# Kernel tuning notes

Hardware: AMD Instinct MI355X
Metric: run time of the kernel (lower is better)

The kernel has to match this reference:

```python
import jax, jax.numpy as jnp
import numpy as np

N = 40000      # nodes
E = 640000     # edges (avg degree 16)
ND = 128       # node_dim
ED = 64        # edge_dim
LN_EPS = 1e-5


def setup_inputs() -> dict:
    key = jax.random.key(0)
    ks = jax.random.split(key, 16)
    s = lambda k, shape, fan_in: jax.random.normal(k, shape, dtype=jnp.float32) * (1.0 / np.sqrt(fan_in))
    return {
        "node_features": jax.random.normal(ks[0], (N, ND), dtype=jnp.float32),
        "edge_indices": jax.random.randint(ks[1], (2, E), 0, N, dtype=jnp.int32),
        "edge_features": jax.random.normal(ks[2], (E, ED), dtype=jnp.float32),
        # message_mlp: Linear(2*ND+ED -> ND), LayerNorm(ND), ReLU, Linear(ND -> ND)
        "W1": s(ks[3], (2 * ND + ED, ND), 2 * ND + ED),
        "b1": jnp.zeros((ND,), jnp.float32),
        "ln_g": jnp.ones((ND,), jnp.float32),
        "ln_b": jnp.zeros((ND,), jnp.float32),
        "W2": s(ks[4], (ND, ND), ND),
        "b2": jnp.zeros((ND,), jnp.float32),
        # edge_gate: Linear(ED -> 1) + Sigmoid
        "gate_w": s(ks[5], (ED, 1), ED),
        "gate_b": jnp.zeros((1,), jnp.float32),
        # GRUCell(ND, ND): weight_ih [3*ND, ND], weight_hh [3*ND, ND] (gates r, z, n)
        "W_ih": s(ks[6], (3 * ND, ND), ND),
        "b_ih": jnp.zeros((3 * ND,), jnp.float32),
        "W_hh": s(ks[7], (3 * ND, ND), ND),
        "b_hh": jnp.zeros((3 * ND,), jnp.float32),
    }


def reference(node_features, edge_indices, edge_features, W1, b1, ln_g, ln_b,
              W2, b2, gate_w, gate_b, W_ih, b_ih, W_hh, b_hh):
    src, dst = edge_indices[0], edge_indices[1]
    # gather src/dst node features and concat with edge features -> [E, 2*ND+ED]
    edge_inputs = jnp.concatenate(
        [node_features[src], node_features[dst], edge_features], axis=1)
    # message MLP: Linear -> LayerNorm -> ReLU -> Linear
    h = edge_inputs @ W1 + b1
    mu = jnp.mean(h, axis=-1, keepdims=True)
    var = jnp.var(h, axis=-1, keepdims=True)
    h = (h - mu) * jax.lax.rsqrt(var + LN_EPS) * ln_g + ln_b
    h = jax.nn.relu(h)
    messages = h @ W2 + b2                                   # [E, ND]
    # sigmoid edge gate from raw edge features
    gate = jax.nn.sigmoid(edge_features @ gate_w + gate_b)   # [E, 1]
    messages = messages * gate
    # scatter-add into destination nodes
    agg = jax.ops.segment_sum(messages, dst, num_segments=node_features.shape[0])
    # GRUCell(input=agg, hidden=node_features), torch gate order: r, z, n
    gi = agg @ W_ih.T + b_ih
    gh = node_features @ W_hh.T + b_hh
    i_r, i_z, i_n = jnp.split(gi, 3, axis=1)
    h_r, h_z, h_n = jnp.split(gh, 3, axis=1)
    r = jax.nn.sigmoid(i_r + h_r)
    z = jax.nn.sigmoid(i_z + h_z)
    n = jnp.tanh(i_n + r * h_n)
    return (1.0 - z) * n + z * node_features
```

## Files before the change

### kernel.cpp

```cpp
#include <hip/hip_runtime.h>
#include <math.h>

#define ND 128
#define ED 64
#define LN_EPS 1e-5f
#define TE 64
#define SXH 328
#define GSH 136
#define GSF 132

typedef _Float16 f16;
typedef __attribute__((ext_vector_type(8))) _Float16 f16x8;
typedef __attribute__((ext_vector_type(4))) _Float16 f16x4;
typedef __attribute__((ext_vector_type(4))) float f32x4;

__device__ __forceinline__ float sigmoidf_(float x) { return 1.f / (1.f + expf(-x)); }

__global__ void convert_kernel(const float* __restrict__ W1, const float* __restrict__ W2,
                               const float* __restrict__ Wih, const float* __restrict__ Whh,
                               f16* __restrict__ W1f, f16* __restrict__ W2f,
                               f16* __restrict__ Wihf, f16* __restrict__ Whhf)
{
    int idx = blockIdx.x * 256 + threadIdx.x;
    if (idx < 40960) {
        int n = idx / 320, k = idx - n * 320;
        W1f[idx] = (f16)W1[k * 128 + n];
    } else if (idx < 57344) {
        int i2 = idx - 40960; int n = i2 >> 7, k = i2 & 127;
        W2f[i2] = (f16)W2[k * 128 + n];
    } else if (idx < 106496) {
        int i3 = idx - 57344;  Wihf[i3] = (f16)Wih[i3];
    } else if (idx < 155648) {
        int i4 = idx - 106496; Whhf[i4] = (f16)Whh[i4];
    }
}

__global__ void nf16_kernel(const float* __restrict__ nf, f16* __restrict__ nf16, int n8) {
    int i = blockIdx.x * 256 + threadIdx.x;
    if (i < n8) {
        float4 a = ((const float4*)nf)[2 * i];
        float4 b = ((const float4*)nf)[2 * i + 1];
        f16x8 h;
        h[0] = (f16)a.x; h[1] = (f16)a.y; h[2] = (f16)a.z; h[3] = (f16)a.w;
        h[4] = (f16)b.x; h[5] = (f16)b.y; h[6] = (f16)b.z; h[7] = (f16)b.w;
        ((f16x8*)nf16)[i] = h;
    }
}

__global__ void hist_kernel(const int* __restrict__ eidx, int* __restrict__ cnt, int E) {
    int i = blockIdx.x * 256 + threadIdx.x;
    if (i < E) atomicAdd(&cnt[eidx[E + i]], 1);
}

__global__ __launch_bounds__(1024)
void scan_kernel(const int* __restrict__ cnt, int* __restrict__ woff, int N) {
    __shared__ int part[1024];
    const int t = threadIdx.x;
    const int CH = 40;
    int base = t * CH;
    int s = 0;
    for (int i = 0; i < CH; ++i) { int idx = base + i; if (idx < N) s += cnt[idx]; }
    part[t] = s;
    __syncthreads();
    for (int d = 1; d < 1024; d <<= 1) {
        int v = (t >= d) ? part[t - d] : 0;
        __syncthreads();
        part[t] += v;
        __syncthreads();
    }
    int run = (t == 0) ? 0 : part[t - 1];
    for (int i = 0; i < CH; ++i) {
        int idx = base + i;
        if (idx < N) { woff[idx] = run; run += cnt[idx]; }
    }
}

__global__ void scatter_kernel(const int* __restrict__ eidx, int* __restrict__ woff,
                               int* __restrict__ perm, int E) {
    int i = blockIdx.x * 256 + threadIdx.x;
    if (i < E) {
        int p = atomicAdd(&woff[eidx[E + i]], 1);
        perm[p] = i;
    }
}

__global__ __launch_bounds__(256, 3)
void edge_kernel(const f16* __restrict__ nf16, const int* __restrict__ eidx,
                 const float* __restrict__ ef, const int* __restrict__ perm,
                 const f16* __restrict__ W1f, const float* __restrict__ b1,
                 const float* __restrict__ ln_g, const float* __restrict__ ln_b,
                 const f16* __restrict__ W2f, const float* __restrict__ b2,
                 const float* __restrict__ gate_w, const float* __restrict__ gate_b,
                 float* __restrict__ agg, int E)
{
    __shared__ f16   sxh[TE * SXH];
    __shared__ float sred[TE * 8];
    __shared__ float spart[TE][4];
    __shared__ float sg[TE];
    __shared__ int   se_s[TE], ssrc_s[TE], sdst_s[TE];

    const int tid  = threadIdx.x;
    const int lane = tid & 63;
    const int w    = __builtin_amdgcn_readfirstlane(tid >> 6);
    const int cb   = 32 * w;
    const int c    = lane & 15;
    const int quad = lane >> 4;
    const int e0   = blockIdx.x * TE;

    if (tid < TE) {
        int e = perm[e0 + tid];
        se_s[tid]   = e;
        ssrc_s[tid] = eidx[e];
        sdst_s[tid] = eidx[E + e];
    }
    __syncthreads();

    {
        const int r = tid >> 2, q = tid & 3;
        const f16*   srow = nf16 + (size_t)ssrc_s[r] * ND;
        const f16*   drow = nf16 + (size_t)sdst_s[r] * ND;
        const float* erow = ef + (size_t)se_s[r] * ED;
        f16* dp = sxh + r * SXH;
        #pragma unroll
        for (int i = 0; i < 4; ++i) {
            int ch = (q + 4 * i) * 8;
            *(f16x8*)(dp + ch)       = *(const f16x8*)(srow + ch);
            *(f16x8*)(dp + 128 + ch) = *(const f16x8*)(drow + ch);
        }
        float gp = 0.f;
        #pragma unroll
        for (int i = 0; i < 4; ++i) {
            int ec = (q + 4 * i) * 4;
            float4 v = *(const float4*)(erow + ec);
            f16x4 h4; h4[0] = (f16)v.x; h4[1] = (f16)v.y; h4[2] = (f16)v.z; h4[3] = (f16)v.w;
            *(f16x4*)(dp + 256 + ec) = h4;
            const float* gw = gate_w + ec;
            gp = fmaf(v.x, gw[0], gp); gp = fmaf(v.y, gw[1], gp);
            gp = fmaf(v.z, gw[2], gp); gp = fmaf(v.w, gw[3], gp);
        }
        spart[r][q] = gp;
    }
    __syncthreads();

    if (tid < TE)
        sg[tid] = sigmoidf_(spart[tid][0] + spart[tid][1] + spart[tid][2] + spart[tid][3] + gate_b[0]);

    f32x4 acc[4][2];
    #pragma unroll
    for (int mt = 0; mt < 4; ++mt)
        #pragma unroll
        for (int nt = 0; nt < 2; ++nt) acc[mt][nt] = (f32x4){0.f, 0.f, 0.f, 0.f};

    #pragma unroll
    for (int ks = 0; ks < 10; ++ks) {
        f16x8 b0 = *(const f16x8*)(W1f + (cb + c) * 320 + ks * 32 + quad * 8);
        f16x8 b1v = *(const f16x8*)(W1f + (cb + 16 + c) * 320 + ks * 32 + quad * 8);
        #pragma unroll
        for (int mt = 0; mt < 4; ++mt) {
            f16x8 a = *(const f16x8*)(sxh + (16 * mt + c) * SXH + ks * 32 + quad * 8);
            acc[mt][0] = __builtin_amdgcn_mfma_f32_16x16x32_f16(a, b0,  acc[mt][0], 0, 0, 0);
            acc[mt][1] = __builtin_amdgcn_mfma_f32_16x16x32_f16(a, b1v, acc[mt][1], 0, 0, 0);
        }
    }

    float b1c[2], gvc[2], bvc[2], b2c[2];
    #pragma unroll
    for (int nt = 0; nt < 2; ++nt) {
        int col = cb + nt * 16 + c;
        b1c[nt] = b1[col]; gvc[nt] = ln_g[col]; bvc[nt] = ln_b[col]; b2c[nt] = b2[col];
    }
    #pragma unroll
    for (int mt = 0; mt < 4; ++mt) {
        float p1[4] = {0, 0, 0, 0}, p2[4] = {0, 0, 0, 0};
        #pragma unroll
        for (int nt = 0; nt < 2; ++nt)
            #pragma unroll
            for (int r = 0; r < 4; ++r) {
                float vv = acc[mt][nt][r] + b1c[nt];
                acc[mt][nt][r] = vv;
                p1[r] += vv; p2[r] += vv * vv;
            }
        #pragma unroll
        for (int m = 1; m < 16; m <<= 1)
            #pragma unroll
            for (int r = 0; r < 4; ++r) {
                p1[r] += __shfl_xor(p1[r], m);
                p2[r] += __shfl_xor(p2[r], m);
            }
        if (c == 0) {
            #pragma unroll
            for (int r = 0; r < 4; ++r) {
                int row = 16 * mt + 4 * quad + r;
                sred[row * 8 + 2 * w + 0] = p1[r];
                sred[row * 8 + 2 * w + 1] = p2[r];
            }
        }
    }
    __syncthreads();

    #pragma unroll
    for (int mt = 0; mt < 4; ++mt)
        #pragma unroll
        for (int r = 0; r < 4; ++r) {
            int row = 16 * mt + 4 * quad + r;
            f32x4 lo = *(const f32x4*)(sred + row * 8);
            f32x4 hi = *(const f32x4*)(sred + row * 8 + 4);
            float t1 = lo[0] + lo[2] + hi[0] + hi[2];
            float t2 = lo[1] + lo[3] + hi[1] + hi[3];
            float mu = t1 * (1.f / 128.f);
            float var = t2 * (1.f / 128.f) - mu * mu;
            float rs = rsqrtf(var + LN_EPS);
            #pragma unroll
            for (int nt = 0; nt < 2; ++nt) {
                float vv = (acc[mt][nt][r] - mu) * rs * gvc[nt] + bvc[nt];
                vv = vv > 0.f ? vv : 0.f;
                sxh[row * SXH + cb + nt * 16 + c] = (f16)vv;
            }
        }
    __syncthreads();

    f32x4 acc2[4][2];
    #pragma unroll
    for (int mt = 0; mt < 4; ++mt)
        #pragma unroll
        for (int nt = 0; nt < 2; ++nt) acc2[mt][nt] = (f32x4){0.f, 0.f, 0.f, 0.f};
    #pragma unroll
    for (int ks = 0; ks < 4; ++ks) {
        f16x8 b0 = *(const f16x8*)(W2f + (cb + c) * 128 + ks * 32 + quad * 8);
        f16x8 b1v = *(const f16x8*)(W2f + (cb + 16 + c) * 128 + ks * 32 + quad * 8);
        #pragma unroll
        for (int mt = 0; mt < 4; ++mt) {
            f16x8 a = *(const f16x8*)(sxh + (16 * mt + c) * SXH + ks * 32 + quad * 8);
            acc2[mt][0] = __builtin_amdgcn_mfma_f32_16x16x32_f16(a, b0,  acc2[mt][0], 0, 0, 0);
            acc2[mt][1] = __builtin_amdgcn_mfma_f32_16x16x32_f16(a, b1v, acc2[mt][1], 0, 0, 0);
        }
    }
    __syncthreads();

    float* smsg = (float*)sxh;
    #pragma unroll
    for (int mt = 0; mt < 4; ++mt)
        #pragma unroll
        for (int r = 0; r < 4; ++r) {
            int row = 16 * mt + 4 * quad + r;
            float gr = sg[row];
            #pragma unroll
            for (int nt = 0; nt < 2; ++nt)
                smsg[row * 164 + cb + nt * 16 + c] = (acc2[mt][nt][r] + b2c[nt]) * gr;
        }
    __syncthreads();

    {
        const int rbase = 16 * w;
        const float* sm = smsg + rbase * 164;
        float run0 = sm[lane];
        float run1 = sm[64 + lane];
        int prev = __builtin_amdgcn_readfirstlane(sdst_s[rbase]);
        #pragma unroll
        for (int r = 1; r < 16; ++r) {
            int d = __builtin_amdgcn_readfirstlane(sdst_s[rbase + r]);
            float v0 = sm[r * 164 + lane];
            float v1 = sm[r * 164 + 64 + lane];
            if (d == prev) { run0 += v0; run1 += v1; }
            else {
                atomicAdd(agg + (size_t)prev * ND + lane,      run0);
                atomicAdd(agg + (size_t)prev * ND + 64 + lane, run1);
                run0 = v0; run1 = v1; prev = d;
            }
        }
        atomicAdd(agg + (size_t)prev * ND + lane,      run0);
        atomicAdd(agg + (size_t)prev * ND + 64 + lane, run1);
    }
}

__global__ __launch_bounds__(256, 2)
void gru_kernel(const float* __restrict__ agg, const float* __restrict__ nf,
                const f16* __restrict__ Wihf, const float* __restrict__ b_ih,
                const f16* __restrict__ Whhf, const float* __restrict__ b_hh,
                float* __restrict__ out)
{
    __shared__ f16   sa[32 * GSH];
    __shared__ f16   sh[32 * GSH];
    __shared__ float shf[32 * GSF];

    const int tid  = threadIdx.x;
    const int lane = tid & 63;
    const int w    = __builtin_amdgcn_readfirstlane(tid >> 6);
    const int c    = lane & 15;
    const int quad = lane >> 4;
    const int n0   = blockIdx.x * 32;

    {
        const int r = tid >> 3, q = tid & 7;
        const float* arow = agg + (size_t)(n0 + r) * ND;
        const float* hrow = nf  + (size_t)(n0 + r) * ND;
        #pragma unroll
        for (int i = 0; i < 4; ++i) {
            int ec = (q + 8 * i) * 4;
            float4 va = *(const float4*)(arow + ec);
            f16x4 ha; ha[0] = (f16)va.x; ha[1] = (f16)va.y; ha[2] = (f16)va.z; ha[3] = (f16)va.w;
            *(f16x4*)(sa + r * GSH + ec) = ha;
            float4 vh = *(const float4*)(hrow + ec);
            f16x4 hh; hh[0] = (f16)vh.x; hh[1] = (f16)vh.y; hh[2] = (f16)vh.z; hh[3] = (f16)vh.w;
            *(f16x4*)(sh + r * GSH + ec) = hh;
            *(float4*)(shf + r * GSF + ec) = vh;
        }
    }
    __syncthreads();

    f32x4 aI[2][6], aH[2][6];
    #pragma unroll
    for (int mt = 0; mt < 2; ++mt)
        #pragma unroll
        for (int j = 0; j < 6; ++j) {
            aI[mt][j] = (f32x4){0.f, 0.f, 0.f, 0.f};
            aH[mt][j] = (f32x4){0.f, 0.f, 0.f, 0.f};
        }

    #pragma unroll
    for (int ks = 0; ks < 4; ++ks) {
        f16x8 fa[2], fh[2];
        #pragma unroll
        for (int mt = 0; mt < 2; ++mt) {
            fa[mt] = *(const f16x8*)(sa + (16 * mt + c) * GSH + ks * 32 + quad * 8);
            fh[mt] = *(const f16x8*)(sh + (16 * mt + c) * GSH + ks * 32 + quad * 8);
        }
        #pragma unroll
        for (int gg = 0; gg < 3; ++gg)
            #pragma unroll
            for (int nt = 0; nt < 2; ++nt) {
                int coln = gg * 128 + 32 * w + nt * 16 + c;
                f16x8 bI = *(const f16x8*)(Wihf + coln * 128 + ks * 32 + quad * 8);
                f16x8 bH = *(const f16x8*)(Whhf + coln * 128 + ks * 32 + quad * 8);
                #pragma unroll
                for (int mt = 0; mt < 2; ++mt) {
                    int j = gg * 2 + nt;
                    aI[mt][j] = __builtin_amdgcn_mfma_f32_16x16x32_f16(fa[mt], bI, aI[mt][j], 0, 0, 0);
                    aH[mt][j] = __builtin_amdgcn_mfma_f32_16x16x32_f16(fh[mt], bH, aH[mt][j], 0, 0, 0);
                }
            }
    }

    #pragma unroll
    for (int nt = 0; nt < 2; ++nt) {
        int col = 32 * w + nt * 16 + c;
        float bir = b_ih[col], biz = b_ih[128 + col], bin = b_ih[256 + col];
        float bhr = b_hh[col], bhz = b_hh[128 + col], bhn = b_hh[256 + col];
        #pragma unroll
        for (int mt = 0; mt < 2; ++mt)
            #pragma unroll
            for (int r = 0; r < 4; ++r) {
                int row = 16 * mt + 4 * quad + r;
                float rr = sigmoidf_(aI[mt][0 + nt][r] + bir + aH[mt][0 + nt][r] + bhr);
                float zz = sigmoidf_(aI[mt][2 + nt][r] + biz + aH[mt][2 + nt][r] + bhz);
                float nn = tanhf(aI[mt][4 + nt][r] + bin + rr * (aH[mt][4 + nt][r] + bhn));
                float hp = shf[row * GSF + col];
                out[(size_t)(n0 + row) * ND + col] = (1.f - zz) * nn + zz * hp;
            }
    }
}

extern "C" void kernel_launch(void* const* d_in, const int* in_sizes, int n_in,
                              void* d_out, int out_size, void* d_ws, size_t ws_size,
                              hipStream_t stream) {
    const float* nf     = (const float*)d_in[0];
    const int*   eidx   = (const int*)  d_in[1];
    const float* ef     = (const float*)d_in[2];
    const float* W1     = (const float*)d_in[3];
    const float* b1     = (const float*)d_in[4];
    const float* ln_g   = (const float*)d_in[5];
    const float* ln_b   = (const float*)d_in[6];
    const float* W2     = (const float*)d_in[7];
    const float* b2     = (const float*)d_in[8];
    const float* gate_w = (const float*)d_in[9];
    const float* gate_b = (const float*)d_in[10];
    const float* W_ih   = (const float*)d_in[11];
    const float* b_ih   = (const float*)d_in[12];
    const float* W_hh   = (const float*)d_in[13];
    const float* b_hh   = (const float*)d_in[14];
    float* out = (float*)d_out;

    const int N = in_sizes[0] / ND;
    const int E = in_sizes[1] / 2;

    char* ws = (char*)d_ws;
    float* agg = (float*)ws;          ws += (size_t)N * ND * 4;
    f16* nf16 = (f16*)ws;             ws += (size_t)N * ND * 2;
    f16* W1f  = (f16*)ws;             ws += 40960 * 2;
    f16* W2f  = (f16*)ws;             ws += 16384 * 2;
    f16* Wihf = (f16*)ws;             ws += 49152 * 2;
    f16* Whhf = (f16*)ws;             ws += 49152 * 2;
    int* cnt  = (int*)ws;             ws += 40960 * 4;
    int* woff = (int*)ws;             ws += 40960 * 4;
    int* perm = (int*)ws;             ws += (size_t)E * 4;

    hipMemsetAsync(agg, 0, (size_t)N * ND * 4, stream);
    hipMemsetAsync(cnt, 0, (size_t)N * 4, stream);
    convert_kernel<<<608, 256, 0, stream>>>(W1, W2, W_ih, W_hh, W1f, W2f, Wihf, Whhf);
    const int n8 = N * ND / 8;
    nf16_kernel<<<(n8 + 255) / 256, 256, 0, stream>>>(nf, nf16, n8);
    hist_kernel<<<(E + 255) / 256, 256, 0, stream>>>(eidx, cnt, E);
    scan_kernel<<<1, 1024, 0, stream>>>(cnt, woff, N);
    scatter_kernel<<<(E + 255) / 256, 256, 0, stream>>>(eidx, woff, perm, E);
    edge_kernel<<<E / TE, 256, 0, stream>>>(nf16, eidx, ef, perm, W1f, b1, ln_g, ln_b,
                                            W2f, b2, gate_w, gate_b, agg, E);
    gru_kernel<<<N / 32, 256, 0, stream>>>(agg, nf, Wihf, b_ih, Whhf, b_hh, out);
}
```

Measured before the change: 611.6 us.

## Halve edge tile, gather node rows via global_load_lds, fuse nf16 conversion into convert

Shrinks the edge tile from 64 to 32 edges per block and raises the occupancy hint from 3 to 5 blocks per SM. Source and destination node rows are now copied straight into LDS with global_load_lds, with indices held in registers and broadcast via readlane instead of staged through shared arrays, which removes one barrier. The node-feature fp16 conversion is folded into the weight-conversion kernel, saving a launch. Smaller tiles mean each W1/W2 fragment loaded from global memory feeds fewer MFMAs, and segmented reduction runs over 8 rows per wave, so more atomics may be issued.

After: 701.3 us. 1.15x slower.

```diff
diff --git a/kernel.cpp b/kernel.cpp
--- a/kernel.cpp
+++ b/kernel.cpp
@@ -4,7 +4,7 @@
 #define ND 128
 #define ED 64
 #define LN_EPS 1e-5f
-#define TE 64
+#define TE 32
 #define SXH 328
 #define GSH 136
 #define GSF 132
@@ -14,12 +14,18 @@
 typedef __attribute__((ext_vector_type(4))) _Float16 f16x4;
 typedef __attribute__((ext_vector_type(4))) float f32x4;
 
+#define GLD4(gp, lp) __builtin_amdgcn_global_load_lds( \
+    (const __attribute__((address_space(1))) void*)(gp), \
+    (__attribute__((address_space(3))) void*)(lp), 4, 0, 0)
+
 __device__ __forceinline__ float sigmoidf_(float x) { return 1.f / (1.f + expf(-x)); }
 
 __global__ void convert_kernel(const float* __restrict__ W1, const float* __restrict__ W2,
                                const float* __restrict__ Wih, const float* __restrict__ Whh,
+                               const float* __restrict__ nf,
                                f16* __restrict__ W1f, f16* __restrict__ W2f,
-                               f16* __restrict__ Wihf, f16* __restrict__ Whhf)
+                               f16* __restrict__ Wihf, f16* __restrict__ Whhf,
+                               f16* __restrict__ nf16, int n8)
 {
     int idx = blockIdx.x * 256 + threadIdx.x;
     if (idx < 40960) {
@@ -32,18 +38,16 @@
         int i3 = idx - 57344;  Wihf[i3] = (f16)Wih[i3];
     } else if (idx < 155648) {
         int i4 = idx - 106496; Whhf[i4] = (f16)Whh[i4];
-    }
-}
-
-__global__ void nf16_kernel(const float* __restrict__ nf, f16* __restrict__ nf16, int n8) {
-    int i = blockIdx.x * 256 + threadIdx.x;
-    if (i < n8) {
-        float4 a = ((const float4*)nf)[2 * i];
-        float4 b = ((const float4*)nf)[2 * i + 1];
-        f16x8 h;
-        h[0] = (f16)a.x; h[1] = (f16)a.y; h[2] = (f16)a.z; h[3] = (f16)a.w;
-        h[4] = (f16)b.x; h[5] = (f16)b.y; h[6] = (f16)b.z; h[7] = (f16)b.w;
-        ((f16x8*)nf16)[i] = h;
+    } else {
+        int i5 = idx - 155648;
+        if (i5 < n8) {
+            float4 a = ((const float4*)nf)[2 * i5];
+            float4 b = ((const float4*)nf)[2 * i5 + 1];
+            f16x8 h;
+            h[0] = (f16)a.x; h[1] = (f16)a.y; h[2] = (f16)a.z; h[3] = (f16)a.w;
+            h[4] = (f16)b.x; h[5] = (f16)b.y; h[6] = (f16)b.z; h[7] = (f16)b.w;
+            ((f16x8*)nf16)[i5] = h;
+        }
     }
 }
 
@@ -84,7 +88,7 @@
     }
 }
 
-__global__ __launch_bounds__(256, 3)
+__global__ __launch_bounds__(256, 5)
 void edge_kernel(const f16* __restrict__ nf16, const int* __restrict__ eidx,
                  const float* __restrict__ ef, const int* __restrict__ perm,
                  const f16* __restrict__ W1f, const float* __restrict__ b1,
@@ -95,9 +99,8 @@
 {
     __shared__ f16   sxh[TE * SXH];
     __shared__ float sred[TE * 8];
-    __shared__ float spart[TE][4];
+    __shared__ float spart[TE][8];
     __shared__ float sg[TE];
-    __shared__ int   se_s[TE], ssrc_s[TE], sdst_s[TE];
 
     const int tid  = threadIdx.x;
     const int lane = tid & 63;
@@ -107,47 +110,52 @@
     const int quad = lane >> 4;
     const int e0   = blockIdx.x * TE;
 
+    int ev = 0, sr = 0, dr = 0;
+    if (lane < 32) {
+        ev = perm[e0 + lane];
+        sr = eidx[ev];
+        dr = eidx[E + ev];
+    }
+
+    #pragma unroll
+    for (int i = 0; i < 8; ++i) {
+        int r = 8 * w + i;
+        int srcr = __builtin_amdgcn_readlane(sr, r);
+        int drr  = __builtin_amdgcn_readlane(dr, r);
+        GLD4(nf16 + (size_t)srcr * ND + 2 * lane, sxh + r * SXH);
+        GLD4(nf16 + (size_t)drr  * ND + 2 * lane, sxh + r * SXH + 128);
+    }
+
+    {
+        const int r = tid >> 3, q = tid & 7;
+        int er = __shfl(ev, r);
+        const float* erow = ef + (size_t)er * ED + q * 8;
+        float4 v0 = *(const float4*)erow;
+        float4 v1 = *(const float4*)(erow + 4);
+        f16x4 h0; h0[0] = (f16)v0.x; h0[1] = (f16)v0.y; h0[2] = (f16)v0.z; h0[3] = (f16)v0.w;
+        f16x4 h1; h1[0] = (f16)v1.x; h1[1] = (f16)v1.y; h1[2] = (f16)v1.z; h1[3] = (f16)v1.w;
+        f16* dp = sxh + r * SXH + 256 + q * 8;
+        *(f16x4*)dp = h0;
+        *(f16x4*)(dp + 4) = h1;
+        const float* gw = gate_w + q * 8;
+        float gp = 0.f;
+        gp = fmaf(v0.x, gw[0], gp); gp = fmaf(v0.y, gw[1], gp);
+        gp = fmaf(v0.z, gw[2], gp); gp = fmaf(v0.w, gw[3], gp);
+        gp = fmaf(v1.x, gw[4], gp); gp = fmaf(v1.y, gw[5], gp);
+        gp = fmaf(v1.z, gw[6], gp); gp = fmaf(v1.w, gw[7], gp);
+        spart[r][q] = gp;
+    }
+    __syncthreads();
+
     if (tid < TE) {
-        int e = perm[e0 + tid];
-        se_s[tid]   = e;
-        ssrc_s[tid] = eidx[e];
-        sdst_s[tid] = eidx[E + e];
-    }
-    __syncthreads();
-
-    {
-        const int r = tid >> 2, q = tid & 3;
-        const f16*   srow = nf16 + (size_t)ssrc_s[r] * ND;
-        const f16*   drow = nf16 + (size_t)sdst_s[r] * ND;
-        const float* erow = ef + (size_t)se_s[r] * ED;
-        f16* dp = sxh + r * SXH;
-        #pragma unroll
-        for (int i = 0; i < 4; ++i) {
-            int ch = (q + 4 * i) * 8;
-            *(f16x8*)(dp + ch)       = *(const f16x8*)(srow + ch);
-            *(f16x8*)(dp + 128 + ch) = *(const f16x8*)(drow + ch);
-        }
-        float gp = 0.f;
-        #pragma unroll
-        for (int i = 0; i < 4; ++i) {
-            int ec = (q + 4 * i) * 4;
-            float4 v = *(const float4*)(erow + ec);
-            f16x4 h4; h4[0] = (f16)v.x; h4[1] = (f16)v.y; h4[2] = (f16)v.z; h4[3] = (f16)v.w;
-            *(f16x4*)(dp + 256 + ec) = h4;
-            const float* gw = gate_w + ec;
-            gp = fmaf(v.x, gw[0], gp); gp = fmaf(v.y, gw[1], gp);
-            gp = fmaf(v.z, gw[2], gp); gp = fmaf(v.w, gw[3], gp);
-        }
-        spart[r][q] = gp;
-    }
-    __syncthreads();
-
-    if (tid < TE)
-        sg[tid] = sigmoidf_(spart[tid][0] + spart[tid][1] + spart[tid][2] + spart[tid][3] + gate_b[0]);
-
-    f32x4 acc[4][2];
-    #pragma unroll
-    for (int mt = 0; mt < 4; ++mt)
+        float s = spart[tid][0] + spart[tid][1] + spart[tid][2] + spart[tid][3]
+                + spart[tid][4] + spart[tid][5] + spart[tid][6] + spart[tid][7];
+        sg[tid] = sigmoidf_(s + gate_b[0]);
+    }
+
+    f32x4 acc[2][2];
+    #pragma unroll
+    for (int mt = 0; mt < 2; ++mt)
         #pragma unroll
         for (int nt = 0; nt < 2; ++nt) acc[mt][nt] = (f32x4){0.f, 0.f, 0.f, 0.f};
 
@@ -156,7 +164,7 @@
         f16x8 b0 = *(const f16x8*)(W1f + (cb + c) * 320 + ks * 32 + quad * 8);
         f16x8 b1v = *(const f16x8*)(W1f + (cb + 16 + c) * 320 + ks * 32 + quad * 8);
         #pragma unroll
-        for (int mt = 0; mt < 4; ++mt) {
+        for (int mt = 0; mt < 2; ++mt) {
             f16x8 a = *(const f16x8*)(sxh + (16 * mt + c) * SXH + ks * 32 + quad * 8);
             acc[mt][0] = __builtin_amdgcn_mfma_f32_16x16x32_f16(a, b0,  acc[mt][0], 0, 0, 0);
             acc[mt][1] = __builtin_amdgcn_mfma_f32_16x16x32_f16(a, b1v, acc[mt][1], 0, 0, 0);
@@ -170,7 +178,7 @@
         b1c[nt] = b1[col]; gvc[nt] = ln_g[col]; bvc[nt] = ln_b[col]; b2c[nt] = b2[col];
     }
     #pragma unroll
-    for (int mt = 0; mt < 4; ++mt) {
+    for (int mt = 0; mt < 2; ++mt) {
         float p1[4] = {0, 0, 0, 0}, p2[4] = {0, 0, 0, 0};
         #pragma unroll
         for (int nt = 0; nt < 2; ++nt)
@@ -199,7 +207,7 @@
     __syncthreads();
 
     #pragma unroll
-    for (int mt = 0; mt < 4; ++mt)
+    for (int mt = 0; mt < 2; ++mt)
         #pragma unroll
         for (int r = 0; r < 4; ++r) {
             int row = 16 * mt + 4 * quad + r;
@@ -219,9 +227,9 @@
         }
     __syncthreads();
 
-    f32x4 acc2[4][2];
-    #pragma unroll
-    for (int mt = 0; mt < 4; ++mt)
+    f32x4 acc2[2][2];
+    #pragma unroll
+    for (int mt = 0; mt < 2; ++mt)
         #pragma unroll
         for (int nt = 0; nt < 2; ++nt) acc2[mt][nt] = (f32x4){0.f, 0.f, 0.f, 0.f};
     #pragma unroll
@@ -229,7 +237,7 @@
         f16x8 b0 = *(const f16x8*)(W2f + (cb + c) * 128 + ks * 32 + quad * 8);
         f16x8 b1v = *(const f16x8*)(W2f + (cb + 16 + c) * 128 + ks * 32 + quad * 8);
         #pragma unroll
-        for (int mt = 0; mt < 4; ++mt) {
+        for (int mt = 0; mt < 2; ++mt) {
             f16x8 a = *(const f16x8*)(sxh + (16 * mt + c) * SXH + ks * 32 + quad * 8);
             acc2[mt][0] = __builtin_amdgcn_mfma_f32_16x16x32_f16(a, b0,  acc2[mt][0], 0, 0, 0);
             acc2[mt][1] = __builtin_amdgcn_mfma_f32_16x16x32_f16(a, b1v, acc2[mt][1], 0, 0, 0);
@@ -239,7 +247,7 @@
 
     float* smsg = (float*)sxh;
     #pragma unroll
-    for (int mt = 0; mt < 4; ++mt)
+    for (int mt = 0; mt < 2; ++mt)
         #pragma unroll
         for (int r = 0; r < 4; ++r) {
             int row = 16 * mt + 4 * quad + r;
@@ -251,14 +259,14 @@
     __syncthreads();
 
     {
-        const int rbase = 16 * w;
+        const int rbase = 8 * w;
         const float* sm = smsg + rbase * 164;
         float run0 = sm[lane];
         float run1 = sm[64 + lane];
-        int prev = __builtin_amdgcn_readfirstlane(sdst_s[rbase]);
-        #pragma unroll
-        for (int r = 1; r < 16; ++r) {
-            int d = __builtin_amdgcn_readfirstlane(sdst_s[rbase + r]);
+        int prev = __builtin_amdgcn_readlane(dr, rbase);
+        #pragma unroll
+        for (int r = 1; r < 8; ++r) {
+            int d = __builtin_amdgcn_readlane(dr, rbase + r);
             float v0 = sm[r * 164 + lane];
             float v1 = sm[r * 164 + 64 + lane];
             if (d == prev) { run0 += v0; run1 += v1; }
@@ -396,9 +404,10 @@
 
     hipMemsetAsync(agg, 0, (size_t)N * ND * 4, stream);
     hipMemsetAsync(cnt, 0, (size_t)N * 4, stream);
-    convert_kernel<<<608, 256, 0, stream>>>(W1, W2, W_ih, W_hh, W1f, W2f, Wihf, Whhf);
     const int n8 = N * ND / 8;
-    nf16_kernel<<<(n8 + 255) / 256, 256, 0, stream>>>(nf, nf16, n8);
+    const int cvt_items = 155648 + n8;
+    convert_kernel<<<(cvt_items + 255) / 256, 256, 0, stream>>>(
+        W1, W2, W_ih, W_hh, nf, W1f, W2f, Wihf, Whhf, nf16, n8);
     hist_kernel<<<(E + 255) / 256, 256, 0, stream>>>(eidx, cnt, E);
     scan_kernel<<<1, 1024, 0, stream>>>(cnt, woff, N);
     scatter_kernel<<<(E + 255) / 256, 256, 0, stream>>>(eidx, woff, perm, E);
```

## Precompute per-node W1 projections to shrink per-edge first GEMM

Applied to the files above, without the earlier changes.

Splits the first linear layer so the src and dst node parts are computed once per node (N×256 f16 table) in a new h12 kernel, and the edge kernel only gathers and sums two projected rows plus a K=64 edge-feature GEMM. This removes most of the per-edge first-layer MFMA work (K 320→64) and the separate nf16 conversion. Shared memory is reorganised with XOR swizzling and shrunk, and occupancy is raised to 4 blocks per CU. The risk is extra f16 rounding, since the projected values are stored in half precision and summed in f16 before the bias and LayerNorm.

After: 562.1 us. 8.1% less time.

```diff
diff --git a/kernel.cpp b/kernel.cpp
--- a/kernel.cpp
+++ b/kernel.cpp
@@ -5,7 +5,6 @@
 #define ED 64
 #define LN_EPS 1e-5f
 #define TE 64
-#define SXH 328
 #define GSH 136
 #define GSF 132
 
@@ -18,32 +17,83 @@
 
 __global__ void convert_kernel(const float* __restrict__ W1, const float* __restrict__ W2,
                                const float* __restrict__ Wih, const float* __restrict__ Whh,
-                               f16* __restrict__ W1f, f16* __restrict__ W2f,
+                               f16* __restrict__ Wcatf, f16* __restrict__ W1ef,
+                               f16* __restrict__ W2f,
                                f16* __restrict__ Wihf, f16* __restrict__ Whhf)
 {
     int idx = blockIdx.x * 256 + threadIdx.x;
-    if (idx < 40960) {
-        int n = idx / 320, k = idx - n * 320;
-        W1f[idx] = (f16)W1[k * 128 + n];
+    if (idx < 32768) {
+        int cc = idx >> 7, k = idx & 127;
+        Wcatf[idx] = (f16)(cc < 128 ? W1[k * 128 + cc] : W1[(128 + k) * 128 + (cc - 128)]);
+    } else if (idx < 40960) {
+        int i2 = idx - 32768; int n = i2 >> 6, k = i2 & 63;
+        W1ef[i2] = (f16)W1[(256 + k) * 128 + n];
     } else if (idx < 57344) {
-        int i2 = idx - 40960; int n = i2 >> 7, k = i2 & 127;
-        W2f[i2] = (f16)W2[k * 128 + n];
+        int i3 = idx - 40960; int n = i3 >> 7, k = i3 & 127;
+        W2f[i3] = (f16)W2[k * 128 + n];
     } else if (idx < 106496) {
-        int i3 = idx - 57344;  Wihf[i3] = (f16)Wih[i3];
+        int i4 = idx - 57344;  Wihf[i4] = (f16)Wih[i4];
     } else if (idx < 155648) {
-        int i4 = idx - 106496; Whhf[i4] = (f16)Whh[i4];
-    }
-}
-
-__global__ void nf16_kernel(const float* __restrict__ nf, f16* __restrict__ nf16, int n8) {
-    int i = blockIdx.x * 256 + threadIdx.x;
-    if (i < n8) {
-        float4 a = ((const float4*)nf)[2 * i];
-        float4 b = ((const float4*)nf)[2 * i + 1];
-        f16x8 h;
-        h[0] = (f16)a.x; h[1] = (f16)a.y; h[2] = (f16)a.z; h[3] = (f16)a.w;
-        h[4] = (f16)b.x; h[5] = (f16)b.y; h[6] = (f16)b.z; h[7] = (f16)b.w;
-        ((f16x8*)nf16)[i] = h;
+        int i5 = idx - 106496; Whhf[i5] = (f16)Whh[i5];
+    }
+}
+
+__global__ __launch_bounds__(256)
+void h12_kernel(const float* __restrict__ nf, const f16* __restrict__ Wcatf,
+                f16* __restrict__ H12f)
+{
+    __shared__ f16 sa[32 * GSH];
+    const int tid  = threadIdx.x;
+    const int lane = tid & 63;
+    const int w    = __builtin_amdgcn_readfirstlane(tid >> 6);
+    const int c    = lane & 15;
+    const int quad = lane >> 4;
+    const int n0   = blockIdx.x * 32;
+
+    {
+        const int r = tid >> 3, q = tid & 7;
+        const float* hrow = nf + (size_t)(n0 + r) * ND;
+        #pragma unroll
+        for (int i = 0; i < 4; ++i) {
+            int ec = (q + 8 * i) * 4;
+            float4 v = *(const float4*)(hrow + ec);
+            f16x4 h; h[0] = (f16)v.x; h[1] = (f16)v.y; h[2] = (f16)v.z; h[3] = (f16)v.w;
+            *(f16x4*)(sa + r * GSH + ec) = h;
+        }
+    }
+    __syncthreads();
+
+    f32x4 acc[2][4];
+    #pragma unroll
+    for (int mt = 0; mt < 2; ++mt)
+        #pragma unroll
+        for (int nt = 0; nt < 4; ++nt) acc[mt][nt] = (f32x4){0.f, 0.f, 0.f, 0.f};
+
+    #pragma unroll
+    for (int ks = 0; ks < 4; ++ks) {
+        f16x8 fa[2];
+        #pragma unroll
+        for (int mt = 0; mt < 2; ++mt)
+            fa[mt] = *(const f16x8*)(sa + (16 * mt + c) * GSH + ks * 32 + quad * 8);
+        #pragma unroll
+        for (int nt = 0; nt < 4; ++nt) {
+            f16x8 b = *(const f16x8*)(Wcatf + (64 * w + nt * 16 + c) * 128 + ks * 32 + quad * 8);
+            #pragma unroll
+            for (int mt = 0; mt < 2; ++mt)
+                acc[mt][nt] = __builtin_amdgcn_mfma_f32_16x16x32_f16(fa[mt], b, acc[mt][nt], 0, 0, 0);
+        }
+    }
+
+    #pragma unroll
+    for (int nt = 0; nt < 4; ++nt) {
+        int col = 64 * w + nt * 16 + c;
+        #pragma unroll
+        for (int mt = 0; mt < 2; ++mt)
+            #pragma unroll
+            for (int r = 0; r < 4; ++r) {
+                int row = 16 * mt + 4 * quad + r;
+                H12f[(size_t)(n0 + row) * 256 + col] = (f16)acc[mt][nt][r];
+            }
     }
 }
 
@@ -84,20 +134,23 @@
     }
 }
 
-__global__ __launch_bounds__(256, 3)
-void edge_kernel(const f16* __restrict__ nf16, const int* __restrict__ eidx,
+__global__ __launch_bounds__(256, 4)
+void edge_kernel(const f16* __restrict__ H12f, const int* __restrict__ eidx,
                  const float* __restrict__ ef, const int* __restrict__ perm,
-                 const f16* __restrict__ W1f, const float* __restrict__ b1,
+                 const f16* __restrict__ W1ef, const float* __restrict__ b1,
                  const float* __restrict__ ln_g, const float* __restrict__ ln_b,
                  const f16* __restrict__ W2f, const float* __restrict__ b2,
                  const float* __restrict__ gate_w, const float* __restrict__ gate_b,
                  float* __restrict__ agg, int E)
 {
-    __shared__ f16   sxh[TE * SXH];
+    __shared__ float smsg[TE * 128];
     __shared__ float sred[TE * 8];
     __shared__ float spart[TE][4];
     __shared__ float sg[TE];
     __shared__ int   se_s[TE], ssrc_s[TE], sdst_s[TE];
+
+    char* shb  = (char*)smsg;
+    char* sefb = (char*)smsg + 16384;
 
     const int tid  = threadIdx.x;
     const int lane = tid & 63;
@@ -117,26 +170,34 @@
 
     {
         const int r = tid >> 2, q = tid & 3;
-        const f16*   srow = nf16 + (size_t)ssrc_s[r] * ND;
-        const f16*   drow = nf16 + (size_t)sdst_s[r] * ND;
+        const f16* h1p = H12f + (size_t)ssrc_s[r] * 256;
+        const f16* h2p = H12f + (size_t)sdst_s[r] * 256 + 128;
+        const int swz = (r & 7) << 4;
+        #pragma unroll
+        for (int i = 0; i < 4; ++i) {
+            int ch = q + 4 * i;
+            f16x8 a = *(const f16x8*)(h1p + ch * 8);
+            f16x8 b = *(const f16x8*)(h2p + ch * 8);
+            f16x8 s = a + b;
+            *(f16x8*)(shb + ((r * 256 + ch * 16) ^ swz)) = s;
+        }
         const float* erow = ef + (size_t)se_s[r] * ED;
-        f16* dp = sxh + r * SXH;
-        #pragma unroll
-        for (int i = 0; i < 4; ++i) {
-            int ch = (q + 4 * i) * 8;
-            *(f16x8*)(dp + ch)       = *(const f16x8*)(srow + ch);
-            *(f16x8*)(dp + 128 + ch) = *(const f16x8*)(drow + ch);
-        }
         float gp = 0.f;
         #pragma unroll
-        for (int i = 0; i < 4; ++i) {
-            int ec = (q + 4 * i) * 4;
-            float4 v = *(const float4*)(erow + ec);
-            f16x4 h4; h4[0] = (f16)v.x; h4[1] = (f16)v.y; h4[2] = (f16)v.z; h4[3] = (f16)v.w;
-            *(f16x4*)(dp + 256 + ec) = h4;
-            const float* gw = gate_w + ec;
-            gp = fmaf(v.x, gw[0], gp); gp = fmaf(v.y, gw[1], gp);
-            gp = fmaf(v.z, gw[2], gp); gp = fmaf(v.w, gw[3], gp);
+        for (int j = 0; j < 2; ++j) {
+            int ch = 2 * q + j;
+            const float* p = erow + ch * 8;
+            float4 v0 = *(const float4*)p;
+            float4 v1 = *(const float4*)(p + 4);
+            f16x8 h;
+            h[0] = (f16)v0.x; h[1] = (f16)v0.y; h[2] = (f16)v0.z; h[3] = (f16)v0.w;
+            h[4] = (f16)v1.x; h[5] = (f16)v1.y; h[6] = (f16)v1.z; h[7] = (f16)v1.w;
+            *(f16x8*)(sefb + ((r * 128 + ch * 16) ^ swz)) = h;
+            const float* gw = gate_w + ch * 8;
+            gp = fmaf(v0.x, gw[0], gp); gp = fmaf(v0.y, gw[1], gp);
+            gp = fmaf(v0.z, gw[2], gp); gp = fmaf(v0.w, gw[3], gp);
+            gp = fmaf(v1.x, gw[4], gp); gp = fmaf(v1.y, gw[5], gp);
+            gp = fmaf(v1.z, gw[6], gp); gp = fmaf(v1.w, gw[7], gp);
         }
         spart[r][q] = gp;
     }
@@ -152,12 +213,12 @@
         for (int nt = 0; nt < 2; ++nt) acc[mt][nt] = (f32x4){0.f, 0.f, 0.f, 0.f};
 
     #pragma unroll
-    for (int ks = 0; ks < 10; ++ks) {
-        f16x8 b0 = *(const f16x8*)(W1f + (cb + c) * 320 + ks * 32 + quad * 8);
-        f16x8 b1v = *(const f16x8*)(W1f + (cb + 16 + c) * 320 + ks * 32 + quad * 8);
+    for (int ks = 0; ks < 2; ++ks) {
+        f16x8 b0 = *(const f16x8*)(W1ef + (cb + c) * 64 + ks * 32 + quad * 8);
+        f16x8 b1v = *(const f16x8*)(W1ef + (cb + 16 + c) * 64 + ks * 32 + quad * 8);
         #pragma unroll
         for (int mt = 0; mt < 4; ++mt) {
-            f16x8 a = *(const f16x8*)(sxh + (16 * mt + c) * SXH + ks * 32 + quad * 8);
+            f16x8 a = *(const f16x8*)(sefb + (((16 * mt + c) * 128 + ks * 64 + quad * 16) ^ ((c & 7) << 4)));
             acc[mt][0] = __builtin_amdgcn_mfma_f32_16x16x32_f16(a, b0,  acc[mt][0], 0, 0, 0);
             acc[mt][1] = __builtin_amdgcn_mfma_f32_16x16x32_f16(a, b1v, acc[mt][1], 0, 0, 0);
         }
@@ -176,7 +237,10 @@
         for (int nt = 0; nt < 2; ++nt)
             #pragma unroll
             for (int r = 0; r < 4; ++r) {
-                float vv = acc[mt][nt][r] + b1c[nt];
+                int row = 16 * mt + 4 * quad + r;
+                int col = cb + nt * 16 + c;
+                float h12v = (float)(*(const f16*)(shb + ((row * 256 + col * 2) ^ ((row & 7) << 4))));
+                float vv = acc[mt][nt][r] + b1c[nt] + h12v;
                 acc[mt][nt][r] = vv;
                 p1[r] += vv; p2[r] += vv * vv;
             }
@@ -212,9 +276,10 @@
             float rs = rsqrtf(var + LN_EPS);
             #pragma unroll
             for (int nt = 0; nt < 2; ++nt) {
+                int col = cb + nt * 16 + c;
                 float vv = (acc[mt][nt][r] - mu) * rs * gvc[nt] + bvc[nt];
                 vv = vv > 0.f ? vv : 0.f;
-                sxh[row * SXH + cb + nt * 16 + c] = (f16)vv;
+                *(f16*)(shb + ((row * 256 + col * 2) ^ ((row & 7) << 4))) = (f16)vv;
             }
         }
     __syncthreads();
@@ -230,14 +295,13 @@
         f16x8 b1v = *(const f16x8*)(W2f + (cb + 16 + c) * 128 + ks * 32 + quad * 8);
         #pragma unroll
         for (int mt = 0; mt < 4; ++mt) {
-            f16x8 a = *(const f16x8*)(sxh + (16 * mt + c) * SXH + ks * 32 + quad * 8);
+            f16x8 a = *(const f16x8*)(shb + (((16 * mt + c) * 256 + ks * 64 + quad * 16) ^ ((c & 7) << 4)));
             acc2[mt][0] = __builtin_amdgcn_mfma_f32_16x16x32_f16(a, b0,  acc2[mt][0], 0, 0, 0);
             acc2[mt][1] = __builtin_amdgcn_mfma_f32_16x16x32_f16(a, b1v, acc2[mt][1], 0, 0, 0);
         }
     }
     __syncthreads();
 
-    float* smsg = (float*)sxh;
     #pragma unroll
     for (int mt = 0; mt < 4; ++mt)
         #pragma unroll
@@ -245,22 +309,25 @@
             int row = 16 * mt + 4 * quad + r;
             float gr = sg[row];
             #pragma unroll
-            for (int nt = 0; nt < 2; ++nt)
-                smsg[row * 164 + cb + nt * 16 + c] = (acc2[mt][nt][r] + b2c[nt]) * gr;
+            for (int nt = 0; nt < 2; ++nt) {
+                int col = cb + nt * 16 + c;
+                smsg[(row * 128 + col) ^ ((row & 7) << 2)] = (acc2[mt][nt][r] + b2c[nt]) * gr;
+            }
         }
     __syncthreads();
 
     {
         const int rbase = 16 * w;
-        const float* sm = smsg + rbase * 164;
-        float run0 = sm[lane];
-        float run1 = sm[64 + lane];
-        int prev = __builtin_amdgcn_readfirstlane(sdst_s[rbase]);
+        int row0 = rbase;
+        float run0 = smsg[(row0 * 128 + lane) ^ ((row0 & 7) << 2)];
+        float run1 = smsg[(row0 * 128 + 64 + lane) ^ ((row0 & 7) << 2)];
+        int prev = sdst_s[rbase];
         #pragma unroll
         for (int r = 1; r < 16; ++r) {
-            int d = __builtin_amdgcn_readfirstlane(sdst_s[rbase + r]);
-            float v0 = sm[r * 164 + lane];
-            float v1 = sm[r * 164 + 64 + lane];
+            int row = rbase + r;
+            int d = sdst_s[row];
+            float v0 = smsg[(row * 128 + lane) ^ ((row & 7) << 2)];
+            float v1 = smsg[(row * 128 + 64 + lane) ^ ((row & 7) << 2)];
             if (d == prev) { run0 += v0; run1 += v1; }
             else {
                 atomicAdd(agg + (size_t)prev * ND + lane,      run0);
@@ -384,25 +451,26 @@
     const int E = in_sizes[1] / 2;
 
     char* ws = (char*)d_ws;
-    float* agg = (float*)ws;          ws += (size_t)N * ND * 4;
-    f16* nf16 = (f16*)ws;             ws += (size_t)N * ND * 2;
-    f16* W1f  = (f16*)ws;             ws += 40960 * 2;
-    f16* W2f  = (f16*)ws;             ws += 16384 * 2;
-    f16* Wihf = (f16*)ws;             ws += 49152 * 2;
-    f16* Whhf = (f16*)ws;             ws += 49152 * 2;
-    int* cnt  = (int*)ws;             ws += 40960 * 4;
-    int* woff = (int*)ws;             ws += 40960 * 4;
-    int* perm = (int*)ws;             ws += (size_t)E * 4;
+    float* agg  = (float*)ws;         ws += (size_t)N * ND * 4;
+    f16* H12f   = (f16*)ws;           ws += (size_t)N * 256 * 2;
+    f16* Wcatf  = (f16*)ws;           ws += 32768 * 2;
+    f16* W1ef   = (f16*)ws;           ws += 8192 * 2;
+    f16* W2f    = (f16*)ws;           ws += 16384 * 2;
+    f16* Wihf   = (f16*)ws;           ws += 49152 * 2;
+    f16* Whhf   = (f16*)ws;           ws += 49152 * 2;
+    int* cnt    = (int*)ws;           ws += 40960 * 4;
+    int* woff   = (int*)ws;           ws += 40960 * 4;
+    int* perm   = (int*)ws;           ws += (size_t)E * 4;
 
     hipMemsetAsync(agg, 0, (size_t)N * ND * 4, stream);
     hipMemsetAsync(cnt, 0, (size_t)N * 4, stream);
-    convert_kernel<<<608, 256, 0, stream>>>(W1, W2, W_ih, W_hh, W1f, W2f, Wihf, Whhf);
-    const int n8 = N * ND / 8;
-    nf16_kernel<<<(n8 + 255) / 256, 256, 0, stream>>>(nf, nf16, n8);
+    convert_kernel<<<608, 256, 0, stream>>>(W1, W2, W_ih, W_hh,
+                                            Wcatf, W1ef, W2f, Wihf, Whhf);
+    h12_kernel<<<N / 32, 256, 0, stream>>>(nf, Wcatf, H12f);
     hist_kernel<<<(E + 255) / 256, 256, 0, stream>>>(eidx, cnt, E);
     scan_kernel<<<1, 1024, 0, stream>>>(cnt, woff, N);
     scatter_kernel<<<(E + 255) / 256, 256, 0, stream>>>(eidx, woff, perm, E);
-    edge_kernel<<<E / TE, 256, 0, stream>>>(nf16, eidx, ef, perm, W1f, b1, ln_g, ln_b,
+    edge_kernel<<<E / TE, 256, 0, stream>>>(H12f, eidx, ef, perm, W1ef, b1, ln_g, ln_b,
                                             W2f, b2, gate_w, gate_b, agg, E);
     gru_kernel<<<N / 32, 256, 0, stream>>>(agg, nf, Wihf, b_ih, Whhf, b_hh, out);
 }
```
